# Performance work log

Hardware: AMD Instinct MI355X
Metric: run time of the kernel (lower is better)

## Reference

```python
import jax, jax.numpy as jnp
import numpy as np

B, N, C, H = 64, 197, 768, 12
D = C // H            # head_dim = 64
P = 14                # patch grid; N = 1 + P*P (cls token + spatial tokens)
FOURIER_SCALE = 1.0


def setup_inputs() -> dict:
    key = jax.random.key(0)
    ks = jax.random.split(key, 6)
    x = jax.random.normal(ks[0], (B, N, C), jnp.float32)
    # Linear weights (torch layout: [out, in]), xavier-ish scaling
    qkv_w = jax.random.normal(ks[1], (3 * C, C), jnp.float32) * np.float32(1.0 / np.sqrt(C))
    wq = jax.random.normal(ks[2], (H, D, D), jnp.float32) * np.float32(np.sqrt(2.0 / (D + D)))
    wk = jax.random.normal(ks[3], (H, D, D), jnp.float32) * np.float32(np.sqrt(2.0 / (D + D)))
    proj_w = jax.random.normal(ks[4], (C, C), jnp.float32) * np.float32(1.0 / np.sqrt(C))
    proj_b = jnp.zeros((C,), jnp.float32)
    return {"x": x, "qkv_w": qkv_w, "wq": wq, "wk": wk, "proj_w": proj_w, "proj_b": proj_b}


def _fft2_tokens(t):
    """2D FFT over the spatial token grid, cls token passed through. t: [B,H,N,D] real."""
    cls_tok = t[:, :, :1, :]                                   # [B,H,1,D]
    sp = t[:, :, 1:, :].reshape(B, H, P, P, D)                 # [B,H,P,P,D]
    spf = jnp.fft.fft2(sp, axes=(2, 3)).reshape(B, H, P * P, D)  # complex
    return jnp.concatenate([cls_tok.astype(spf.dtype), spf], axis=2)  # [B,H,N,D] complex


def reference(x, qkv_w, wq, wk, proj_w, proj_b):
    # qkv projection (no bias)
    qkv = jnp.einsum('bnc,oc->bno', x, qkv_w)                  # [B,N,3C]
    qkv = qkv.reshape(B, N, 3, H, D).transpose(2, 0, 3, 1, 4)  # [3,B,H,N,D]
    q, k, v = qkv[0], qkv[1], qkv[2]

    # per-head learned Fourier weights
    qt = jnp.einsum('bhnd,hde->bhne', q, wq)
    kt = jnp.einsum('bhnd,hde->bhne', k, wk)

    qf = _fft2_tokens(qt)
    kf = _fft2_tokens(kt)

    # spectral score: Re(q_fft * conj(k_fft)) summed over head_dim -> [B,H,N]
    attn = jnp.real(qf * jnp.conj(kf)).sum(-1) * FOURIER_SCALE
    attn = jax.nn.softmax(attn, axis=-1)                       # softmax over tokens

    # per-token scalar weighting of v (eval mode: dropout is identity)
    out = attn[..., None] * v                                   # [B,H,N,D]
    out = out.transpose(0, 2, 1, 3).reshape(B, N, C)
    return jnp.einsum('bnc,oc->bno', out, proj_w) + proj_b
```

## Files before the change

### kernel.cpp

```cpp
#include <hip/hip_runtime.h>

typedef _Float16 f16;
typedef __attribute__((ext_vector_type(8))) _Float16 f16x8;
typedef __attribute__((ext_vector_type(4))) float f32x4;

__device__ __forceinline__ void gll16(const void* g, void* l) {
  __builtin_amdgcn_global_load_lds((const __attribute__((address_space(1))) void*)g,
                                   (__attribute__((address_space(3))) void*)l, 16, 0, 0);
}

struct alignas(8) H4 { f16 a, b, c, d; };

template <int MODE>
__global__ __launch_bounds__(256, (MODE == 0) ? 2 : 3)
void gemm_nt(const f16* __restrict__ Ah, const f16* __restrict__ Al,
             const f16* __restrict__ Wh, const f16* __restrict__ Wl,
             void* __restrict__ Cp, const float* __restrict__ extra,
             int M, int K, int ldc, int ntiles) {
  constexpr int BUF = (MODE == 0) ? 32768 : 16384;
  constexpr int BO  = (MODE == 0) ? 16384 : 8192;
  __shared__ alignas(16) char lds[2 * BUF];
  const int tid = threadIdx.x;
  const int w = tid >> 6;
  const int lane = tid & 63;

  const int nwg = gridDim.x;
  const int orig = blockIdx.x;
  const int qq = nwg >> 3, rr = nwg & 7;
  const int xcd = orig & 7;
  const int wid = (xcd < rr ? xcd * (qq + 1) : rr * (qq + 1) + (xcd - rr) * qq) + (orig >> 3);
  const int bm = (wid / ntiles) * 128;
  const int bn = (wid % ntiles) * 128;

  f32x4 accA[4][4] = {};
  f32x4 accB[4][4];
  if constexpr (MODE == 0) {
#pragma unroll
    for (int i = 0; i < 4; ++i)
#pragma unroll
      for (int j = 0; j < 4; ++j) accB[i][j] = f32x4{0.f, 0.f, 0.f, 0.f};
  }

  const int srow = tid >> 2;
  const int gslot = (tid & 3) ^ ((srow & 3) ^ ((srow >> 2) & 3));
  int ar0 = bm + srow;      if (ar0 > M - 1) ar0 = M - 1;
  int ar1 = bm + 64 + srow; if (ar1 > M - 1) ar1 = M - 1;
  const f16* pAh0 = Ah + (size_t)ar0 * K + gslot * 8;
  const f16* pAh1 = Ah + (size_t)ar1 * K + gslot * 8;
  const f16* pBh0 = Wh + (size_t)(bn + srow) * K + gslot * 8;
  const f16* pBh1 = Wh + (size_t)(bn + 64 + srow) * K + gslot * 8;
  const f16* pAl0 = nullptr; const f16* pAl1 = nullptr;
  const f16* pBl0 = nullptr; const f16* pBl1 = nullptr;
  if constexpr (MODE == 0) {
    pAl0 = Al + (size_t)ar0 * K + gslot * 8;
    pAl1 = Al + (size_t)ar1 * K + gslot * 8;
    pBl0 = Wl + (size_t)(bn + srow) * K + gslot * 8;
    pBl1 = Wl + (size_t)(bn + 64 + srow) * K + gslot * 8;
  }
  const int wb = w << 10;

  const int fr = lane & 15;
  const int g = lane >> 4;
  const int wm = (w >> 1) * 64;
  const int wn = (w & 1) * 64;
  int aoff[4], boff[4];
#pragma unroll
  for (int i = 0; i < 4; ++i) {
    int row = wm + i * 16 + fr;
    aoff[i] = row * 64 + ((g ^ ((row & 3) ^ ((row >> 2) & 3))) * 16);
    int col = wn + i * 16 + fr;
    boff[i] = col * 64 + ((g ^ ((col & 3) ^ ((col >> 2) & 3))) * 16);
  }

  auto STAGE = [&](int bufo, int kt) {
    char* dst = lds + bufo;
    gll16(pAh0 + kt, dst + wb);
    gll16(pAh1 + kt, dst + 4096 + wb);
    gll16(pBh0 + kt, dst + BO + wb);
    gll16(pBh1 + kt, dst + BO + 4096 + wb);
    if constexpr (MODE == 0) {
      gll16(pAl0 + kt, dst + 8192 + wb);
      gll16(pAl1 + kt, dst + 12288 + wb);
      gll16(pBl0 + kt, dst + BO + 8192 + wb);
      gll16(pBl1 + kt, dst + BO + 12288 + wb);
    }
  };

  auto COMPUTE = [&](int bufo) {
    const char* base = lds + bufo;
    f16x8 ah[4], bh[4];
#pragma unroll
    for (int i = 0; i < 4; ++i) ah[i] = *(const f16x8*)(base + aoff[i]);
#pragma unroll
    for (int j = 0; j < 4; ++j) bh[j] = *(const f16x8*)(base + BO + boff[j]);
#pragma unroll
    for (int i = 0; i < 4; ++i)
#pragma unroll
      for (int j = 0; j < 4; ++j)
        accA[i][j] = __builtin_amdgcn_mfma_f32_16x16x32_f16(ah[i], bh[j], accA[i][j], 0, 0, 0);
    if constexpr (MODE == 0) {
      f16x8 bl[4];
#pragma unroll
      for (int j = 0; j < 4; ++j) bl[j] = *(const f16x8*)(base + BO + 8192 + boff[j]);
#pragma unroll
      for (int i = 0; i < 4; ++i)
#pragma unroll
        for (int j = 0; j < 4; ++j)
          accB[i][j] = __builtin_amdgcn_mfma_f32_16x16x32_f16(ah[i], bl[j], accB[i][j], 0, 0, 0);
      f16x8 al[4];
#pragma unroll
      for (int i = 0; i < 4; ++i) al[i] = *(const f16x8*)(base + 8192 + aoff[i]);
#pragma unroll
      for (int i = 0; i < 4; ++i)
#pragma unroll
        for (int j = 0; j < 4; ++j)
          accB[i][j] = __builtin_amdgcn_mfma_f32_16x16x32_f16(al[i], bh[j], accB[i][j], 0, 0, 0);
    }
  };

  STAGE(0, 0);
  __syncthreads();
  const int nk = K >> 5;
  for (int t = 0; t < nk; ++t) {
    const int cur = (t & 1) ? BUF : 0;
    if (t + 1 < nk) STAGE(cur ^ BUF, (t + 1) << 5);
    COMPUTE(cur);
    __syncthreads();
  }

#pragma unroll
  for (int i = 0; i < 4; ++i) {
#pragma unroll
    for (int j = 0; j < 4; ++j) {
#pragma unroll
      for (int r = 0; r < 4; ++r) {
        int row = bm + wm + i * 16 + g * 4 + r;
        int col = bn + wn + j * 16 + fr;
        if (row < M) {
          float v = accA[i][j][r];
          if constexpr (MODE == 0) {
            v += accB[i][j][r] * (1.0f / 4096.0f);
            ((float*)Cp)[(size_t)row * ldc + col] = v;
          } else if constexpr (MODE == 1) {
            int b = row / 197;
            int n = row - b * 197;
            int hh = col >> 6;
            float aw = extra[(size_t)(b * 12 + hh) * 197 + n];
            ((f16*)Cp)[(size_t)row * ldc + col] = (f16)(aw * v);
          } else {
            ((float*)Cp)[(size_t)row * ldc + col] = v + extra[col];
          }
        }
      }
    }
  }
}

__global__ __launch_bounds__(256) void prep_misc(const float* __restrict__ x,
                                                 const float* __restrict__ qkv_w,
                                                 const float* __restrict__ proj_w,
                                                 f16* __restrict__ Ah, f16* __restrict__ Al,
                                                 f16* __restrict__ Wh, f16* __restrict__ Pw) {
  const int X4 = 2420736;
  const int V4 = 147456;
  int i = blockIdx.x * 256 + threadIdx.x;
  if (i < X4) {
    float4 v = ((const float4*)x)[i];
    H4 hi, lo;
    hi.a = (f16)v.x; hi.b = (f16)v.y; hi.c = (f16)v.z; hi.d = (f16)v.w;
    lo.a = (f16)((v.x - (float)hi.a) * 4096.f);
    lo.b = (f16)((v.y - (float)hi.b) * 4096.f);
    lo.c = (f16)((v.z - (float)hi.c) * 4096.f);
    lo.d = (f16)((v.w - (float)hi.d) * 4096.f);
    ((H4*)Ah)[i] = hi; ((H4*)Al)[i] = lo;
  } else if (i < X4 + V4) {
    int j = i - X4;
    float4 v = ((const float4*)(qkv_w + (size_t)1536 * 768))[j];
    H4 h; h.a = (f16)v.x; h.b = (f16)v.y; h.c = (f16)v.z; h.d = (f16)v.w;
    ((H4*)(Wh + (size_t)1536 * 768))[j] = h;
  } else if (i < X4 + 2 * V4) {
    int j = i - X4 - V4;
    float4 v = ((const float4*)proj_w)[j];
    H4 h; h.a = (f16)v.x; h.b = (f16)v.y; h.c = (f16)v.z; h.d = (f16)v.w;
    ((H4*)Pw)[j] = h;
  }
}

__global__ __launch_bounds__(256) void fold_w(const float* __restrict__ qkv_w,
                                              const float* __restrict__ wq,
                                              const float* __restrict__ wk,
                                              f16* __restrict__ Wh, f16* __restrict__ Wl) {
  const int blk = blockIdx.x;
  const int s = blk / 768;
  const int he = blk - s * 768;
  const int h = he >> 6, e = he & 63;
  const int t = threadIdx.x;
  __shared__ float wv[64];
  if (t < 64) {
    const float* w = (s == 0) ? wq : wk;
    wv[t] = w[(size_t)(h * 64 + t) * 64 + e];
  }
  __syncthreads();
  const float* base = qkv_w + (size_t)(s * 768 + h * 64) * 768;
  float acc0 = 0.f, acc1 = 0.f, acc2 = 0.f;
#pragma unroll 8
  for (int d = 0; d < 64; ++d) {
    float w = wv[d];
    const float* rowp = base + (size_t)d * 768;
    acc0 += w * rowp[t];
    acc1 += w * rowp[t + 256];
    acc2 += w * rowp[t + 512];
  }
  size_t ro = (size_t)blk * 768;
  f16 h0 = (f16)acc0, h1 = (f16)acc1, h2 = (f16)acc2;
  Wh[ro + t]       = h0; Wl[ro + t]       = (f16)((acc0 - (float)h0) * 4096.f);
  Wh[ro + t + 256] = h1; Wl[ro + t + 256] = (f16)((acc1 - (float)h1) * 4096.f);
  Wh[ro + t + 512] = h2; Wl[ro + t + 512] = (f16)((acc2 - (float)h2) * 4096.f);
}

__device__ constexpr float CS14[14] = {
  1.0f,  0.90096886790241915f,  0.62348980185873359f,  0.22252093395631440f,
 -0.22252093395631440f, -0.62348980185873359f, -0.90096886790241915f, -1.0f,
 -0.90096886790241915f, -0.62348980185873359f, -0.22252093395631440f,
  0.22252093395631440f,  0.62348980185873359f,  0.90096886790241915f };
__device__ constexpr float SN14[14] = {
  0.0f, -0.43388373911755823f, -0.78183148246802980f, -0.97492791218182362f,
 -0.97492791218182362f, -0.78183148246802980f, -0.43388373911755823f,  0.0f,
  0.43388373911755823f,  0.78183148246802980f,  0.97492791218182362f,
  0.97492791218182362f,  0.78183148246802980f,  0.43388373911755823f };

template <int F1>
__device__ __forceinline__ float colprod(const float (&qr)[14], const float (&qi)[14],
                                         const float (&kr)[14], const float (&ki)[14]) {
  float qfr = 0.f, qfi = 0.f, kfr = 0.f, kfi = 0.f;
#pragma unroll
  for (int r = 0; r < 14; ++r) {
    const float c = CS14[(r * F1) % 14], s = SN14[(r * F1) % 14];
    qfr += qr[r] * c - qi[r] * s;
    qfi += qr[r] * s + qi[r] * c;
    kfr += kr[r] * c - ki[r] * s;
    kfi += kr[r] * s + ki[r] * c;
  }
  return qfr * kfr + qfi * kfi;
}

__global__ __launch_bounds__(256, 5) void fourier_logits(const float* __restrict__ Cq,
                                                         float* __restrict__ attn_part) {
  const int bid = blockIdx.x;
  const int bh = bid % 768;
  const int chunk = bid / 768;
  const int b = bh / 12, h = bh - b * 12;
  const int t = threadIdx.x;

  __shared__ float qt_s[8][201], kt_s[8][201];
  __shared__ float QRr[8][8][15], QRi[8][8][15], KRr[8][8][15], KRi[8][8][15];

  const float* baseq = Cq + (size_t)(b * 197) * 1536 + h * 64 + chunk * 8;
  for (int i = t; i < 197 * 8; i += 256) {
    int e = i & 7, n = i >> 3;
    qt_s[e][n] = baseq[(size_t)n * 1536 + e];
    kt_s[e][n] = baseq[(size_t)n * 1536 + 768 + e];
  }
  __syncthreads();

  {
    const int qk = t >> 7, e = (t >> 4) & 7, r = t & 15;
    if (r < 14) {
      const float* src = (qk ? kt_s[e] : qt_s[e]) + 1 + r * 14;
      float x[14];
#pragma unroll
      for (int s = 0; s < 14; ++s) x[s] = src[s];
      float (*Rr)[15] = qk ? KRr[e] : QRr[e];
      float (*Ri)[15] = qk ? KRi[e] : QRi[e];
#pragma unroll
      for (int f2 = 0; f2 < 8; ++f2) {
        float re = 0.f, im = 0.f;
#pragma unroll
        for (int s = 0; s < 14; ++s) {
          re += x[s] * CS14[(s * f2) % 14];
          im += x[s] * SN14[(s * f2) % 14];
        }
        Rr[f2][r] = re;
        Ri[f2][r] = im;
      }
    }
  }
  __syncthreads();

  {
    const int f1g = t >> 6, f2 = (t >> 3) & 7, e = t & 7;
    float qr[14], qi[14], kr[14], ki[14];
#pragma unroll
    for (int r = 0; r < 14; ++r) {
      qr[r] = QRr[e][f2][r]; qi[r] = QRi[e][f2][r];
      kr[r] = KRr[e][f2][r]; ki[r] = KRi[e][f2][r];
    }
    float* out = attn_part + (size_t)chunk * 151296 + (size_t)bh * 197;
    auto emit = [&](int f1, float L) {
      L += __shfl_xor(L, 1, 64);
      L += __shfl_xor(L, 2, 64);
      L += __shfl_xor(L, 4, 64);
      if (e == 0) {
        out[1 + f1 * 14 + f2] = L;
        if (f2 >= 1 && f2 <= 6) out[1 + ((14 - f1) % 14) * 14 + (14 - f2)] = L;
      }
    };
    if (f1g == 0) {
      emit(0, colprod<0>(qr, qi, kr, ki));
      emit(1, colprod<1>(qr, qi, kr, ki));
      emit(2, colprod<2>(qr, qi, kr, ki));
      emit(3, colprod<3>(qr, qi, kr, ki));
    } else if (f1g == 1) {
      emit(4, colprod<4>(qr, qi, kr, ki));
      emit(5, colprod<5>(qr, qi, kr, ki));
      emit(6, colprod<6>(qr, qi, kr, ki));
      emit(7, colprod<7>(qr, qi, kr, ki));
    } else if (f1g == 2) {
      emit(8, colprod<8>(qr, qi, kr, ki));
      emit(9, colprod<9>(qr, qi, kr, ki));
      emit(10, colprod<10>(qr, qi, kr, ki));
    } else {
      emit(11, colprod<11>(qr, qi, kr, ki));
      emit(12, colprod<12>(qr, qi, kr, ki));
      emit(13, colprod<13>(qr, qi, kr, ki));
    }
    if (t < 8) {
      float cls = qt_s[t][0] * kt_s[t][0];
      cls += __shfl_xor(cls, 1, 64);
      cls += __shfl_xor(cls, 2, 64);
      cls += __shfl_xor(cls, 4, 64);
      if (t == 0) out[0] = cls;
    }
  }
}

__global__ __launch_bounds__(64) void softmax_k(const float* __restrict__ ap,
                                                float* __restrict__ aw) {
  const int bh = blockIdx.x;
  const int l = threadIdx.x;
  float v[4];
#pragma unroll
  for (int j = 0; j < 4; ++j) {
    int n = j * 64 + l;
    float s = -1e30f;
    if (n < 197) {
      s = 0.f;
#pragma unroll
      for (int c = 0; c < 8; ++c) s += ap[(size_t)c * 151296 + (size_t)bh * 197 + n];
    }
    v[j] = s;
  }
  float m = fmaxf(fmaxf(v[0], v[1]), fmaxf(v[2], v[3]));
#pragma unroll
  for (int o = 32; o; o >>= 1) m = fmaxf(m, __shfl_xor(m, o, 64));
  float e[4];
  float sum = 0.f;
#pragma unroll
  for (int j = 0; j < 4; ++j) {
    int n = j * 64 + l;
    e[j] = (n < 197) ? expf(v[j] - m) : 0.f;
    sum += e[j];
  }
#pragma unroll
  for (int o = 32; o; o >>= 1) sum += __shfl_xor(sum, o, 64);
  float inv = 1.f / sum;
#pragma unroll
  for (int j = 0; j < 4; ++j) {
    int n = j * 64 + l;
    if (n < 197) aw[(size_t)bh * 197 + n] = e[j] * inv;
  }
}

extern "C" void kernel_launch(void* const* d_in, const int* in_sizes, int n_in,
                              void* d_out, int out_size, void* d_ws, size_t ws_size,
                              hipStream_t stream) {
  const float* x      = (const float*)d_in[0];
  const float* qkv_w  = (const float*)d_in[1];
  const float* wq     = (const float*)d_in[2];
  const float* wk     = (const float*)d_in[3];
  const float* proj_w = (const float*)d_in[4];
  const float* proj_b = (const float*)d_in[5];

  char* ws = (char*)d_ws;
  float* Cq     = (float*)ws;
  f16*   Ah     = (f16*)(ws + 77463552);
  f16*   Al     = (f16*)(ws + 96829440);
  f16*   Wh     = (f16*)(ws + 116195328);
  f16*   Wl     = (f16*)(ws + 119734272);
  f16*   Pw     = (f16*)(ws + 122093568);
  float* attn_p = (float*)(ws + 123273216);
  float* attn_w = (float*)(ws + 128114688);
  f16*   out_pre= (f16*)(ws + 128719872);

  prep_misc<<<10608, 256, 0, stream>>>(x, qkv_w, proj_w, Ah, Al, Wh, Pw);
  fold_w<<<1536, 256, 0, stream>>>(qkv_w, wq, wk, Wh, Wl);
  gemm_nt<0><<<1188, 256, 0, stream>>>(Ah, Al, Wh, Wl, Cq, nullptr, 12608, 768, 1536, 12);
  fourier_logits<<<6144, 256, 0, stream>>>(Cq, attn_p);
  softmax_k<<<768, 64, 0, stream>>>(attn_p, attn_w);
  gemm_nt<1><<<594, 256, 0, stream>>>(Ah, nullptr, Wh + (size_t)1536 * 768, nullptr,
                                      out_pre, attn_w, 12608, 768, 768, 6);
  gemm_nt<2><<<594, 256, 0, stream>>>(out_pre, nullptr, Pw, nullptr,
                                      d_out, proj_b, 12608, 768, 768, 6);
}
```

Baseline: 245.8 us.

## Load GEMM A operand directly into registers and merge prep and fold kernels

The GEMM no longer stages the A tile through LDS. Each lane now loads its MFMA A fragments straight from global memory into registers, double-buffered, while only the B tile goes through global_load_lds. This halves the LDS footprint per block and cuts LDS traffic, and it replaces __syncthreads with an explicit vmcnt wait plus barrier. The cost is uncoalesced per-lane 16-byte global loads and duplicated A reads across the two wave columns. Separately, the weight-folding kernel is merged into the prep kernel to save one launch.

```diff
diff --git a/kernel.cpp b/kernel.cpp
--- a/kernel.cpp
+++ b/kernel.cpp
@@ -8,6 +8,8 @@
   __builtin_amdgcn_global_load_lds((const __attribute__((address_space(1))) void*)g,
                                    (__attribute__((address_space(3))) void*)l, 16, 0, 0);
 }
+
+#define WAITVM0() asm volatile("s_waitcnt vmcnt(0)" ::: "memory")
 
 struct alignas(8) H4 { f16 a, b, c, d; };
 
@@ -17,8 +19,7 @@
              const f16* __restrict__ Wh, const f16* __restrict__ Wl,
              void* __restrict__ Cp, const float* __restrict__ extra,
              int M, int K, int ldc, int ntiles) {
-  constexpr int BUF = (MODE == 0) ? 32768 : 16384;
-  constexpr int BO  = (MODE == 0) ? 16384 : 8192;
+  constexpr int BUF = (MODE == 0) ? 16384 : 8192;
   __shared__ alignas(16) char lds[2 * BUF];
   const int tid = threadIdx.x;
   const int w = tid >> 6;
@@ -43,17 +44,10 @@
 
   const int srow = tid >> 2;
   const int gslot = (tid & 3) ^ ((srow & 3) ^ ((srow >> 2) & 3));
-  int ar0 = bm + srow;      if (ar0 > M - 1) ar0 = M - 1;
-  int ar1 = bm + 64 + srow; if (ar1 > M - 1) ar1 = M - 1;
-  const f16* pAh0 = Ah + (size_t)ar0 * K + gslot * 8;
-  const f16* pAh1 = Ah + (size_t)ar1 * K + gslot * 8;
   const f16* pBh0 = Wh + (size_t)(bn + srow) * K + gslot * 8;
   const f16* pBh1 = Wh + (size_t)(bn + 64 + srow) * K + gslot * 8;
-  const f16* pAl0 = nullptr; const f16* pAl1 = nullptr;
   const f16* pBl0 = nullptr; const f16* pBl1 = nullptr;
   if constexpr (MODE == 0) {
-    pAl0 = Al + (size_t)ar0 * K + gslot * 8;
-    pAl1 = Al + (size_t)ar1 * K + gslot * 8;
     pBl0 = Wl + (size_t)(bn + srow) * K + gslot * 8;
     pBl1 = Wl + (size_t)(bn + 64 + srow) * K + gslot * 8;
   }
@@ -63,36 +57,43 @@
   const int g = lane >> 4;
   const int wm = (w >> 1) * 64;
   const int wn = (w & 1) * 64;
-  int aoff[4], boff[4];
+  int boff[4];
+#pragma unroll
+  for (int j = 0; j < 4; ++j) {
+    int col = wn + j * 16 + fr;
+    boff[j] = col * 64 + ((g ^ ((col & 3) ^ ((col >> 2) & 3))) * 16);
+  }
+  const f16* pArow[4];
 #pragma unroll
   for (int i = 0; i < 4; ++i) {
-    int row = wm + i * 16 + fr;
-    aoff[i] = row * 64 + ((g ^ ((row & 3) ^ ((row >> 2) & 3))) * 16);
-    int col = wn + i * 16 + fr;
-    boff[i] = col * 64 + ((g ^ ((col & 3) ^ ((col >> 2) & 3))) * 16);
-  }
-
-  auto STAGE = [&](int bufo, int kt) {
+    int row = bm + wm + i * 16 + fr; if (row > M - 1) row = M - 1;
+    pArow[i] = Ah + (size_t)row * K + g * 8;
+  }
+  const size_t loDelta = (MODE == 0) ? (size_t)(Al - Ah) : 0;
+
+  auto STAGEB = [&](int bufo, int kt) {
     char* dst = lds + bufo;
-    gll16(pAh0 + kt, dst + wb);
-    gll16(pAh1 + kt, dst + 4096 + wb);
-    gll16(pBh0 + kt, dst + BO + wb);
-    gll16(pBh1 + kt, dst + BO + 4096 + wb);
+    gll16(pBh0 + kt, dst + wb);
+    gll16(pBh1 + kt, dst + 4096 + wb);
     if constexpr (MODE == 0) {
-      gll16(pAl0 + kt, dst + 8192 + wb);
-      gll16(pAl1 + kt, dst + 12288 + wb);
-      gll16(pBl0 + kt, dst + BO + 8192 + wb);
-      gll16(pBl1 + kt, dst + BO + 12288 + wb);
+      gll16(pBl0 + kt, dst + 8192 + wb);
+      gll16(pBl1 + kt, dst + 12288 + wb);
     }
   };
 
-  auto COMPUTE = [&](int bufo) {
+  auto LOADA = [&](f16x8 (&h)[4], f16x8 (&l)[4], int kt) {
+#pragma unroll
+    for (int i = 0; i < 4; ++i) {
+      h[i] = *(const f16x8*)(pArow[i] + kt);
+      if constexpr (MODE == 0) l[i] = *(const f16x8*)(pArow[i] + loDelta + kt);
+    }
+  };
+
+  auto COMPUTE = [&](int bufo, f16x8 (&ah)[4], f16x8 (&al)[4]) {
     const char* base = lds + bufo;
-    f16x8 ah[4], bh[4];
-#pragma unroll
-    for (int i = 0; i < 4; ++i) ah[i] = *(const f16x8*)(base + aoff[i]);
-#pragma unroll
-    for (int j = 0; j < 4; ++j) bh[j] = *(const f16x8*)(base + BO + boff[j]);
+    f16x8 bh[4];
+#pragma unroll
+    for (int j = 0; j < 4; ++j) bh[j] = *(const f16x8*)(base + boff[j]);
 #pragma unroll
     for (int i = 0; i < 4; ++i)
 #pragma unroll
@@ -101,15 +102,12 @@
     if constexpr (MODE == 0) {
       f16x8 bl[4];
 #pragma unroll
-      for (int j = 0; j < 4; ++j) bl[j] = *(const f16x8*)(base + BO + 8192 + boff[j]);
+      for (int j = 0; j < 4; ++j) bl[j] = *(const f16x8*)(base + 8192 + boff[j]);
 #pragma unroll
       for (int i = 0; i < 4; ++i)
 #pragma unroll
         for (int j = 0; j < 4; ++j)
           accB[i][j] = __builtin_amdgcn_mfma_f32_16x16x32_f16(ah[i], bl[j], accB[i][j], 0, 0, 0);
-      f16x8 al[4];
-#pragma unroll
-      for (int i = 0; i < 4; ++i) al[i] = *(const f16x8*)(base + 8192 + aoff[i]);
 #pragma unroll
       for (int i = 0; i < 4; ++i)
 #pragma unroll
@@ -118,14 +116,23 @@
     }
   };
 
-  STAGE(0, 0);
-  __syncthreads();
+  f16x8 ahP[4], alP[4], ahQ[4], alQ[4];
   const int nk = K >> 5;
-  for (int t = 0; t < nk; ++t) {
-    const int cur = (t & 1) ? BUF : 0;
-    if (t + 1 < nk) STAGE(cur ^ BUF, (t + 1) << 5);
-    COMPUTE(cur);
-    __syncthreads();
+  STAGEB(0, 0);
+  LOADA(ahP, alP, 0);
+  WAITVM0();
+  __builtin_amdgcn_s_barrier();
+  for (int tp = 0; tp < nk; tp += 2) {
+    if (tp + 1 < nk) { STAGEB(BUF, (tp + 1) << 5); LOADA(ahQ, alQ, (tp + 1) << 5); }
+    COMPUTE(0, ahP, alP);
+    WAITVM0();
+    __builtin_amdgcn_s_barrier();
+    if (tp + 2 < nk) { STAGEB(0, (tp + 2) << 5); LOADA(ahP, alP, (tp + 2) << 5); }
+    if (tp + 1 < nk) {
+      COMPUTE(BUF, ahQ, alQ);
+      WAITVM0();
+      __builtin_amdgcn_s_barrier();
+    }
   }
 
 #pragma unroll
@@ -156,14 +163,46 @@
   }
 }
 
-__global__ __launch_bounds__(256) void prep_misc(const float* __restrict__ x,
+__global__ __launch_bounds__(256) void prep_fold(const float* __restrict__ x,
                                                  const float* __restrict__ qkv_w,
+                                                 const float* __restrict__ wq,
+                                                 const float* __restrict__ wk,
                                                  const float* __restrict__ proj_w,
                                                  f16* __restrict__ Ah, f16* __restrict__ Al,
-                                                 f16* __restrict__ Wh, f16* __restrict__ Pw) {
+                                                 f16* __restrict__ Wh, f16* __restrict__ Wl,
+                                                 f16* __restrict__ Pw) {
+  __shared__ float wv[64];
+  const int t = threadIdx.x;
+  if (blockIdx.x < 1536) {
+    const int blk = blockIdx.x;
+    const int s = blk / 768;
+    const int he = blk - s * 768;
+    const int h = he >> 6, e = he & 63;
+    if (t < 64) {
+      const float* w = (s == 0) ? wq : wk;
+      wv[t] = w[(size_t)(h * 64 + t) * 64 + e];
+    }
+    __syncthreads();
+    const float* base = qkv_w + (size_t)(s * 768 + h * 64) * 768;
+    float acc0 = 0.f, acc1 = 0.f, acc2 = 0.f;
+#pragma unroll 8
+    for (int d = 0; d < 64; ++d) {
+      float w = wv[d];
+      const float* rowp = base + (size_t)d * 768;
+      acc0 += w * rowp[t];
+      acc1 += w * rowp[t + 256];
+      acc2 += w * rowp[t + 512];
+    }
+    size_t ro = (size_t)blk * 768;
+    f16 h0 = (f16)acc0, h1 = (f16)acc1, h2 = (f16)acc2;
+    Wh[ro + t]       = h0; Wl[ro + t]       = (f16)((acc0 - (float)h0) * 4096.f);
+    Wh[ro + t + 256] = h1; Wl[ro + t + 256] = (f16)((acc1 - (float)h1) * 4096.f);
+    Wh[ro + t + 512] = h2; Wl[ro + t + 512] = (f16)((acc2 - (float)h2) * 4096.f);
+    return;
+  }
   const int X4 = 2420736;
   const int V4 = 147456;
-  int i = blockIdx.x * 256 + threadIdx.x;
+  int i = (blockIdx.x - 1536) * 256 + t;
   if (i < X4) {
     float4 v = ((const float4*)x)[i];
     H4 hi, lo;
@@ -184,38 +223,6 @@
     H4 h; h.a = (f16)v.x; h.b = (f16)v.y; h.c = (f16)v.z; h.d = (f16)v.w;
     ((H4*)Pw)[j] = h;
   }
-}
-
-__global__ __launch_bounds__(256) void fold_w(const float* __restrict__ qkv_w,
-                                              const float* __restrict__ wq,
-                                              const float* __restrict__ wk,
-                                              f16* __restrict__ Wh, f16* __restrict__ Wl) {
-  const int blk = blockIdx.x;
-  const int s = blk / 768;
-  const int he = blk - s * 768;
-  const int h = he >> 6, e = he & 63;
-  const int t = threadIdx.x;
-  __shared__ float wv[64];
-  if (t < 64) {
-    const float* w = (s == 0) ? wq : wk;
-    wv[t] = w[(size_t)(h * 64 + t) * 64 + e];
-  }
-  __syncthreads();
-  const float* base = qkv_w + (size_t)(s * 768 + h * 64) * 768;
-  float acc0 = 0.f, acc1 = 0.f, acc2 = 0.f;
-#pragma unroll 8
-  for (int d = 0; d < 64; ++d) {
-    float w = wv[d];
-    const float* rowp = base + (size_t)d * 768;
-    acc0 += w * rowp[t];
-    acc1 += w * rowp[t + 256];
-    acc2 += w * rowp[t + 512];
-  }
-  size_t ro = (size_t)blk * 768;
-  f16 h0 = (f16)acc0, h1 = (f16)acc1, h2 = (f16)acc2;
-  Wh[ro + t]       = h0; Wl[ro + t]       = (f16)((acc0 - (float)h0) * 4096.f);
-  Wh[ro + t + 256] = h1; Wl[ro + t + 256] = (f16)((acc1 - (float)h1) * 4096.f);
-  Wh[ro + t + 512] = h2; Wl[ro + t + 512] = (f16)((acc2 - (float)h2) * 4096.f);
 }
 
 __device__ constexpr float CS14[14] = {
@@ -392,8 +399,7 @@
   float* attn_w = (float*)(ws + 128114688);
   f16*   out_pre= (f16*)(ws + 128719872);
 
-  prep_misc<<<10608, 256, 0, stream>>>(x, qkv_w, proj_w, Ah, Al, Wh, Pw);
-  fold_w<<<1536, 256, 0, stream>>>(qkv_w, wq, wk, Wh, Wl);
+  prep_fold<<<12144, 256, 0, stream>>>(x, qkv_w, wq, wk, proj_w, Ah, Al, Wh, Wl, Pw);
   gemm_nt<0><<<1188, 256, 0, stream>>>(Ah, Al, Wh, Wl, Cq, nullptr, 12608, 768, 1536, 12);
   fourier_logits<<<6144, 256, 0, stream>>>(Cq, attn_p);
   softmax_k<<<768, 64, 0, stream>>>(attn_p, attn_w);
```

Result: slower. 390.2 us (+58.7%).

## Fuse softmax into V-GEMM epilogue and merge prep with weight folding

Applied to the files above, without the earlier changes.

Removes the standalone softmax kernel. Each V-projection GEMM block now recomputes the softmax for the (batch, head) pairs its tile covers and stages the weights in LDS for the epilogue scaling. Also merges the fold_w and prep_misc kernels into one launch. Together these cut two launches and the attn_w round trip, at the cost of redundant softmax work across tiles that share a (batch, head) pair. The LDS indexing assumes a 128-row tile spans at most two batches and that the two head columns map to warp pairs.

```diff
diff --git a/kernel.cpp b/kernel.cpp
--- a/kernel.cpp
+++ b/kernel.cpp
@@ -128,6 +128,47 @@
     __syncthreads();
   }
 
+  const int b_first = bm / 197;
+  if constexpr (MODE == 1) {
+    float* law = (float*)lds;
+    const int bi = w >> 1, hi = w & 1;
+    int bb = b_first + bi; if (bb > 63) bb = 63;
+    const int hh = (bn >> 6) + hi;
+    const float* ap = extra + (size_t)(bb * 12 + hh) * 197;
+    float v4[4];
+#pragma unroll
+    for (int j = 0; j < 4; ++j) {
+      int n = j * 64 + lane;
+      float s = -1e30f;
+      if (n < 197) {
+        s = 0.f;
+#pragma unroll
+        for (int c = 0; c < 8; ++c) s += ap[(size_t)c * 151296 + n];
+      }
+      v4[j] = s;
+    }
+    float m = fmaxf(fmaxf(v4[0], v4[1]), fmaxf(v4[2], v4[3]));
+#pragma unroll
+    for (int o = 32; o; o >>= 1) m = fmaxf(m, __shfl_xor(m, o, 64));
+    float e4[4];
+    float sum = 0.f;
+#pragma unroll
+    for (int j = 0; j < 4; ++j) {
+      int n = j * 64 + lane;
+      e4[j] = (n < 197) ? expf(v4[j] - m) : 0.f;
+      sum += e4[j];
+    }
+#pragma unroll
+    for (int o = 32; o; o >>= 1) sum += __shfl_xor(sum, o, 64);
+    float inv = 1.f / sum;
+#pragma unroll
+    for (int j = 0; j < 4; ++j) {
+      int n = j * 64 + lane;
+      if (n < 197) law[w * 200 + n] = e4[j] * inv;
+    }
+    __syncthreads();
+  }
+
 #pragma unroll
   for (int i = 0; i < 4; ++i) {
 #pragma unroll
@@ -144,8 +185,8 @@
           } else if constexpr (MODE == 1) {
             int b = row / 197;
             int n = row - b * 197;
-            int hh = col >> 6;
-            float aw = extra[(size_t)(b * 12 + hh) * 197 + n];
+            int bi2 = b - b_first;
+            float aw = ((const float*)lds)[(bi2 * 2 + (w & 1)) * 200 + n];
             ((f16*)Cp)[(size_t)row * ldc + col] = (f16)(aw * v);
           } else {
             ((float*)Cp)[(size_t)row * ldc + col] = v + extra[col];
@@ -156,14 +197,46 @@
   }
 }
 
-__global__ __launch_bounds__(256) void prep_misc(const float* __restrict__ x,
+__global__ __launch_bounds__(256) void prep_fold(const float* __restrict__ x,
                                                  const float* __restrict__ qkv_w,
+                                                 const float* __restrict__ wq,
+                                                 const float* __restrict__ wk,
                                                  const float* __restrict__ proj_w,
                                                  f16* __restrict__ Ah, f16* __restrict__ Al,
-                                                 f16* __restrict__ Wh, f16* __restrict__ Pw) {
+                                                 f16* __restrict__ Wh, f16* __restrict__ Wl,
+                                                 f16* __restrict__ Pw) {
+  __shared__ float wv[64];
+  const int t = threadIdx.x;
+  if (blockIdx.x < 1536) {
+    const int blk = blockIdx.x;
+    const int s = blk / 768;
+    const int he = blk - s * 768;
+    const int h = he >> 6, e = he & 63;
+    if (t < 64) {
+      const float* w = (s == 0) ? wq : wk;
+      wv[t] = w[(size_t)(h * 64 + t) * 64 + e];
+    }
+    __syncthreads();
+    const float* base = qkv_w + (size_t)(s * 768 + h * 64) * 768;
+    float acc0 = 0.f, acc1 = 0.f, acc2 = 0.f;
+#pragma unroll 8
+    for (int d = 0; d < 64; ++d) {
+      float w = wv[d];
+      const float* rowp = base + (size_t)d * 768;
+      acc0 += w * rowp[t];
+      acc1 += w * rowp[t + 256];
+      acc2 += w * rowp[t + 512];
+    }
+    size_t ro = (size_t)blk * 768;
+    f16 h0 = (f16)acc0, h1 = (f16)acc1, h2 = (f16)acc2;
+    Wh[ro + t]       = h0; Wl[ro + t]       = (f16)((acc0 - (float)h0) * 4096.f);
+    Wh[ro + t + 256] = h1; Wl[ro + t + 256] = (f16)((acc1 - (float)h1) * 4096.f);
+    Wh[ro + t + 512] = h2; Wl[ro + t + 512] = (f16)((acc2 - (float)h2) * 4096.f);
+    return;
+  }
   const int X4 = 2420736;
   const int V4 = 147456;
-  int i = blockIdx.x * 256 + threadIdx.x;
+  int i = (blockIdx.x - 1536) * 256 + t;
   if (i < X4) {
     float4 v = ((const float4*)x)[i];
     H4 hi, lo;
@@ -184,38 +257,6 @@
     H4 h; h.a = (f16)v.x; h.b = (f16)v.y; h.c = (f16)v.z; h.d = (f16)v.w;
     ((H4*)Pw)[j] = h;
   }
-}
-
-__global__ __launch_bounds__(256) void fold_w(const float* __restrict__ qkv_w,
-                                              const float* __restrict__ wq,
-                                              const float* __restrict__ wk,
-                                              f16* __restrict__ Wh, f16* __restrict__ Wl) {
-  const int blk = blockIdx.x;
-  const int s = blk / 768;
-  const int he = blk - s * 768;
-  const int h = he >> 6, e = he & 63;
-  const int t = threadIdx.x;
-  __shared__ float wv[64];
-  if (t < 64) {
-    const float* w = (s == 0) ? wq : wk;
-    wv[t] = w[(size_t)(h * 64 + t) * 64 + e];
-  }
-  __syncthreads();
-  const float* base = qkv_w + (size_t)(s * 768 + h * 64) * 768;
-  float acc0 = 0.f, acc1 = 0.f, acc2 = 0.f;
-#pragma unroll 8
-  for (int d = 0; d < 64; ++d) {
-    float w = wv[d];
-    const float* rowp = base + (size_t)d * 768;
-    acc0 += w * rowp[t];
-    acc1 += w * rowp[t + 256];
-    acc2 += w * rowp[t + 512];
-  }
-  size_t ro = (size_t)blk * 768;
-  f16 h0 = (f16)acc0, h1 = (f16)acc1, h2 = (f16)acc2;
-  Wh[ro + t]       = h0; Wl[ro + t]       = (f16)((acc0 - (float)h0) * 4096.f);
-  Wh[ro + t + 256] = h1; Wl[ro + t + 256] = (f16)((acc1 - (float)h1) * 4096.f);
-  Wh[ro + t + 512] = h2; Wl[ro + t + 512] = (f16)((acc2 - (float)h2) * 4096.f);
 }
 
 __device__ constexpr float CS14[14] = {
@@ -334,43 +375,6 @@
   }
 }
 
-__global__ __launch_bounds__(64) void softmax_k(const float* __restrict__ ap,
-                                                float* __restrict__ aw) {
-  const int bh = blockIdx.x;
-  const int l = threadIdx.x;
-  float v[4];
-#pragma unroll
-  for (int j = 0; j < 4; ++j) {
-    int n = j * 64 + l;
-    float s = -1e30f;
-    if (n < 197) {
-      s = 0.f;
-#pragma unroll
-      for (int c = 0; c < 8; ++c) s += ap[(size_t)c * 151296 + (size_t)bh * 197 + n];
-    }
-    v[j] = s;
-  }
-  float m = fmaxf(fmaxf(v[0], v[1]), fmaxf(v[2], v[3]));
-#pragma unroll
-  for (int o = 32; o; o >>= 1) m = fmaxf(m, __shfl_xor(m, o, 64));
-  float e[4];
-  float sum = 0.f;
-#pragma unroll
-  for (int j = 0; j < 4; ++j) {
-    int n = j * 64 + l;
-    e[j] = (n < 197) ? expf(v[j] - m) : 0.f;
-    sum += e[j];
-  }
-#pragma unroll
-  for (int o = 32; o; o >>= 1) sum += __shfl_xor(sum, o, 64);
-  float inv = 1.f / sum;
-#pragma unroll
-  for (int j = 0; j < 4; ++j) {
-    int n = j * 64 + l;
-    if (n < 197) aw[(size_t)bh * 197 + n] = e[j] * inv;
-  }
-}
-
 extern "C" void kernel_launch(void* const* d_in, const int* in_sizes, int n_in,
                               void* d_out, int out_size, void* d_ws, size_t ws_size,
                               hipStream_t stream) {
@@ -389,16 +393,13 @@
   f16*   Wl     = (f16*)(ws + 119734272);
   f16*   Pw     = (f16*)(ws + 122093568);
   float* attn_p = (float*)(ws + 123273216);
-  float* attn_w = (float*)(ws + 128114688);
   f16*   out_pre= (f16*)(ws + 128719872);
 
-  prep_misc<<<10608, 256, 0, stream>>>(x, qkv_w, proj_w, Ah, Al, Wh, Pw);
-  fold_w<<<1536, 256, 0, stream>>>(qkv_w, wq, wk, Wh, Wl);
+  prep_fold<<<12144, 256, 0, stream>>>(x, qkv_w, wq, wk, proj_w, Ah, Al, Wh, Wl, Pw);
   gemm_nt<0><<<1188, 256, 0, stream>>>(Ah, Al, Wh, Wl, Cq, nullptr, 12608, 768, 1536, 12);
   fourier_logits<<<6144, 256, 0, stream>>>(Cq, attn_p);
-  softmax_k<<<768, 64, 0, stream>>>(attn_p, attn_w);
   gemm_nt<1><<<594, 256, 0, stream>>>(Ah, nullptr, Wh + (size_t)1536 * 768, nullptr,
-                                      out_pre, attn_w, 12608, 768, 768, 6);
+                                      out_pre, attn_p, 12608, 768, 768, 6);
   gemm_nt<2><<<594, 256, 0, stream>>>(out_pre, nullptr, Pw, nullptr,
                                       d_out, proj_b, 12608, 768, 768, 6);
 }
```

New measurement: 233.0 us. -5.2%, faster.
